# Kernel tuning notes

Measured on AMD Instinct MI355X. Metric: run time of the kernel, lower is better.

The kernel has to match this reference:

```python
import jax, jax.numpy as jnp
import numpy as np

B = 64; WIN_IN = 32; WIN_OUT = 8; NODES = 128; FEAT = 16
HID = 64; LSTM_H = 32; CLASSES = 10
N = B * WIN_IN * NODES      # 262144 total nodes in batched graph
E = 8 * N                   # 2097152 edges (avg degree 8)


def setup_inputs() -> dict:
    key = jax.random.key(0)
    ks = jax.random.split(key, 16)
    p = lambda k, s: (jax.random.normal(k, s, dtype=jnp.float32) * 0.05)
    return {
        "x": jax.random.normal(ks[0], (N, FEAT), dtype=jnp.float32),
        "edge_index": jax.random.randint(ks[1], (2, E), 0, N, dtype=jnp.int32),
        "W1": p(ks[2], (FEAT, HID)),   "b1": p(ks[3], (HID,)),
        "W2": p(ks[4], (HID, FEAT)),   "b2": p(ks[5], (FEAT,)),
        "Wih": p(ks[6], (4 * LSTM_H, NODES * FEAT)),
        "Whh": p(ks[7], (4 * LSTM_H, LSTM_H)),
        "bih": p(ks[8], (4 * LSTM_H,)), "bhh": p(ks[9], (4 * LSTM_H,)),
        "Wfc1": p(ks[10], (16, LSTM_H)), "bfc1": p(ks[11], (16,)),
        "Wfc2": p(ks[12], (CLASSES, 16)), "bfc2": p(ks[13], (CLASSES,)),
    }


def _gcn_conv(x, row, col, W, b):
    # PyG GCNConv: x' = D^-1/2 (A+I) D^-1/2 (x W) + b, deg counted at target (col)
    h = x @ W
    deg = jax.ops.segment_sum(jnp.ones(row.shape[0], jnp.float32), col, num_segments=N) + 1.0
    dinv = jax.lax.rsqrt(deg)
    msg = h[row] * (dinv[row] * dinv[col])[:, None]          # [E, F]
    agg = jax.ops.segment_sum(msg, col, num_segments=N)
    agg = agg + h * (dinv * dinv)[:, None]                   # self-loop term
    return agg + b


def _lstm(seq, Wih, Whh, bih, bhh):
    # seq: [B, T, D] -> outputs [B, T, H]; torch gate order i, f, g, o
    xs = jnp.transpose(seq, (1, 0, 2))
    h0 = jnp.zeros((seq.shape[0], LSTM_H), seq.dtype)
    bias = bih + bhh

    def step(carry, xt):
        h, c = carry
        g = xt @ Wih.T + h @ Whh.T + bias
        i, f, gg, o = jnp.split(g, 4, axis=-1)
        c = jax.nn.sigmoid(f) * c + jax.nn.sigmoid(i) * jnp.tanh(gg)
        h = jax.nn.sigmoid(o) * jnp.tanh(c)
        return (h, c), h

    _, hs = jax.lax.scan(step, (h0, h0), xs)
    return jnp.transpose(hs, (1, 0, 2))


def reference(x, edge_index, W1, b1, W2, b2, Wih, Whh, bih, bhh, Wfc1, bfc1, Wfc2, bfc2):
    row, col = edge_index[0], edge_index[1]
    h = jax.nn.relu(_gcn_conv(x, row, col, W1, b1))
    h = jax.nn.relu(_gcn_conv(h, row, col, W2, b2))
    h = h.reshape(B, WIN_IN, NODES * FEAT)
    h = _lstm(h, Wih, Whh, bih, bhh)
    h = h[:, -WIN_OUT:, :]
    h = jax.nn.relu(h @ Wfc1.T + bfc1)
    h = h @ Wfc2.T + bfc2
    return h.reshape(-1, CLASSES)
```

## Files before the change

### kernel.cpp

```cpp
#include <hip/hip_runtime.h>
#include <hip/hip_fp16.h>

#define NN      262144
#define EDGES   2097152
#define FEATD   16
#define HIDD    64
#define LSTMH   32
#define BATCH   64
#define WIN     32
#define WOUT    8
#define NCLS    10
#define ROWD    2048
#define KCHUNKS 16

#define NB2     512
#define NW      512
#define CAPB    4608
#define NBLK    256
#define CHUNK   (EDGES / NBLK)

__global__ void k_hist(const int* __restrict__ ei, int* __restrict__ hist2d) {
    __shared__ int h[NB2];
    int blk = blockIdx.x, tid = threadIdx.x;
    for (int l = tid; l < NB2; l += 256) h[l] = 0;
    __syncthreads();
    int e0 = blk * CHUNK;
    for (int i = tid; i < CHUNK; i += 256)
        atomicAdd(&h[ei[EDGES + e0 + i] >> 9], 1);
    __syncthreads();
    for (int l = tid; l < NB2; l += 256) hist2d[l * NBLK + blk] = h[l];
}

__global__ void k_scan2(int* __restrict__ hist2d, int* __restrict__ bcnt) {
    __shared__ int s[NBLK];
    int b = blockIdx.x, tid = threadIdx.x;
    int v = hist2d[b * NBLK + tid];
    s[tid] = v;
    __syncthreads();
    for (int off = 1; off < NBLK; off <<= 1) {
        int t = (tid >= off) ? s[tid - off] : 0;
        __syncthreads();
        s[tid] += t;
        __syncthreads();
    }
    hist2d[b * NBLK + tid] = s[tid] - v;
    if (tid == NBLK - 1) bcnt[b] = s[tid];
}

__global__ void k_place(const int* __restrict__ ei, const int* __restrict__ hist2d,
                        int* __restrict__ bdata) {
    __shared__ int curp[NB2];
    int blk = blockIdx.x, tid = threadIdx.x;
    for (int l = tid; l < NB2; l += 256) curp[l] = hist2d[l * NBLK + blk];
    __syncthreads();
    int e0 = blk * CHUNK;
    for (int i = tid; i < CHUNK; i += 256) {
        int r = ei[e0 + i];
        int c = ei[EDGES + e0 + i];
        int b = c >> 9;
        int p = atomicAdd(&curp[b], 1);
        if (p < CAPB) bdata[(size_t)b * CAPB + p] = (r << 9) | (c & 511);
    }
}

__global__ void __launch_bounds__(256)
k_csrsort(const int* __restrict__ bcnt, const int* __restrict__ bdata,
          int* __restrict__ rows, int* __restrict__ off, float* __restrict__ dinv) {
    __shared__ int sidx[CAPB];
    __shared__ int hist[NW], curp[NW];
    int b = blockIdx.x, tid = threadIdx.x;
    int total = bcnt[b]; if (total > CAPB) total = CAPB;
    for (int l = tid; l < NW; l += 256) hist[l] = 0;
    __syncthreads();
    const int* base = bdata + (size_t)b * CAPB;
    for (int i = tid; i < total; i += 256) {
        int w = base[i];
        sidx[i] = w;
        atomicAdd(&hist[w & 511], 1);
    }
    __syncthreads();
    if (tid == 0) {
        int run = 0;
        for (int co = 0; co < NW; co++) { curp[co] = run; run += hist[co]; }
    }
    __syncthreads();
    for (int l = tid; l < NW; l += 256) {
        off[b * NW + l] = curp[l] + hist[l];
        dinv[b * NW + l] = rsqrtf((float)hist[l] + 1.0f);
    }
    __syncthreads();
    for (int i = tid; i < total; i += 256) {
        int w = sidx[i];
        int pos = atomicAdd(&curp[w & 511], 1);
        rows[(size_t)b * CAPB + pos] = w >> 9;
    }
}

__global__ void k_scale(const float* __restrict__ x, const float* __restrict__ dinv,
                        __half2* __restrict__ xsH) {
    int i = blockIdx.x * blockDim.x + threadIdx.x;
    if (i >= NN * 8) return;
    float d = dinv[i >> 3];
    float2 v = ((const float2*)x)[i];
    xsH[i] = __floats2half2_rn(v.x * d, v.y * d);
}

template<int LAYER>
__global__ void __launch_bounds__(256)
k_aggcsr(const int* __restrict__ rows, const int* __restrict__ off,
         const float* __restrict__ dinv, const __half2* __restrict__ srcH,
         const float* __restrict__ b2, __half2* __restrict__ outH) {
    int i = blockIdx.x * blockDim.x + threadIdx.x;
    if (i >= NN * 8) return;
    int n = i >> 3, f2 = i & 7;
    int begin = (n & 511) ? off[n - 1] : 0;
    int end = off[n];
    const size_t base = (size_t)(n >> 9) * CAPB;
    float2 selfv = __half22float2(srcH[(size_t)n * 8 + f2]);
    float ax = selfv.x, ay = selfv.y;
    for (size_t e = base + begin; e < base + end; ++e) {
        int r = rows[e];
        float2 v = __half22float2(srcH[(size_t)r * 8 + f2]);
        ax += v.x; ay += v.y;
    }
    float d = dinv[n];
    ax *= d; ay *= d;
    if (LAYER == 2) {
        ax = fmaxf(ax + b2[f2 * 2 + 0], 0.f);
        ay = fmaxf(ay + b2[f2 * 2 + 1], 0.f);
    }
    outH[i] = __floats2half2_rn(ax, ay);
}

__global__ void k_gcnmlp(const __half2* __restrict__ in1H, __half2* __restrict__ xsH,
                         const float* __restrict__ dinv,
                         const float* __restrict__ W1, const float* __restrict__ b1,
                         const float* __restrict__ W2) {
    __shared__ float sW1[FEATD * HIDD];
    __shared__ float sW2[HIDD * FEATD];
    __shared__ float sb1[HIDD];
    for (int l = threadIdx.x; l < FEATD * HIDD; l += blockDim.x) {
        sW1[l] = W1[l];
        sW2[l] = W2[l];
    }
    if (threadIdx.x < HIDD) sb1[threadIdx.x] = b1[threadIdx.x];
    __syncthreads();
    int n = blockIdx.x * blockDim.x + threadIdx.x;
    if (n >= NN) return;
    union { float4 f4; __half2 h2[4]; } a0, a1;
    a0.f4 = ((const float4*)(in1H + (size_t)n * 8))[0];
    a1.f4 = ((const float4*)(in1H + (size_t)n * 8))[1];
    float in[FEATD];
#pragma unroll
    for (int q = 0; q < 4; q++) {
        float2 v = __half22float2(a0.h2[q]);
        in[q * 2 + 0] = v.x; in[q * 2 + 1] = v.y;
        v = __half22float2(a1.h2[q]);
        in[8 + q * 2 + 0] = v.x; in[8 + q * 2 + 1] = v.y;
    }
    float out[FEATD];
#pragma unroll
    for (int c = 0; c < FEATD; c++) out[c] = 0.f;
#pragma unroll 8
    for (int j = 0; j < HIDD; j++) {
        float h = sb1[j];
#pragma unroll
        for (int f = 0; f < FEATD; f++) h += in[f] * sW1[f * HIDD + j];
        h = fmaxf(h, 0.f);
#pragma unroll
        for (int c = 0; c < FEATD; c++) out[c] += h * sW2[j * FEATD + c];
    }
    float dn = dinv[n];
    union { float4 f4; __half2 h2[4]; } o0, o1;
#pragma unroll
    for (int q = 0; q < 4; q++) {
        o0.h2[q] = __floats2half2_rn(out[q * 2] * dn, out[q * 2 + 1] * dn);
        o1.h2[q] = __floats2half2_rn(out[8 + q * 2] * dn, out[8 + q * 2 + 1] * dn);
    }
    ((float4*)(xsH + (size_t)n * 8))[0] = o0.f4;
    ((float4*)(xsH + (size_t)n * 8))[1] = o1.f4;
}

#define KT 32
#define KSPAN (ROWD / KCHUNKS)
__global__ void __launch_bounds__(256)
k_gemmA(const __half2* __restrict__ h2H, const float* __restrict__ Wih,
        float* __restrict__ gxp) {
    __shared__ float As[16][KT + 2];
    __shared__ float Bs[KT][128 + 4];
    int tid = threadIdx.x;
    int row0 = blockIdx.x * 16;
    int k0 = blockIdx.y * KSPAN;
    int lrow = tid & 15;
    int cb = (tid >> 4) * 8;
    float acc[8];
#pragma unroll
    for (int j = 0; j < 8; j++) acc[j] = 0.f;
    const __half* h2 = (const __half*)h2H;
    for (int kk = 0; kk < KSPAN; kk += KT) {
        if (tid < 64) {
            int rr = tid >> 2, cc = (tid & 3) * 8;
            union { float4 f4; __half2 h2v[4]; } a;
            a.f4 = *(const float4*)(h2 + (size_t)(row0 + rr) * ROWD + k0 + kk + cc);
#pragma unroll
            for (int q = 0; q < 4; q++) {
                float2 v = __half22float2(a.h2v[q]);
                As[rr][cc + q * 2 + 0] = v.x;
                As[rr][cc + q * 2 + 1] = v.y;
            }
        }
#pragma unroll
        for (int w = 0; w < 4; w++) {
            int idx = tid + w * 256;
            int rr = idx >> 3;
            int cc = (idx & 7) * 4;
            float4 v = *(const float4*)&Wih[(size_t)rr * ROWD + k0 + kk + cc];
            Bs[cc + 0][rr] = v.x;
            Bs[cc + 1][rr] = v.y;
            Bs[cc + 2][rr] = v.z;
            Bs[cc + 3][rr] = v.w;
        }
        __syncthreads();
#pragma unroll
        for (int k = 0; k < KT; k++) {
            float a = As[lrow][k];
            float4 b0 = *(const float4*)&Bs[k][cb];
            float4 b1 = *(const float4*)&Bs[k][cb + 4];
            acc[0] += a * b0.x; acc[1] += a * b0.y;
            acc[2] += a * b0.z; acc[3] += a * b0.w;
            acc[4] += a * b1.x; acc[5] += a * b1.y;
            acc[6] += a * b1.z; acc[7] += a * b1.w;
        }
        __syncthreads();
    }
    float* outp = gxp + (size_t)blockIdx.y * (ROWD * 128) + (size_t)(row0 + lrow) * 128 + cb;
    ((float4*)outp)[0] = make_float4(acc[0], acc[1], acc[2], acc[3]);
    ((float4*)outp)[1] = make_float4(acc[4], acc[5], acc[6], acc[7]);
}

__global__ void k_pre(const float* __restrict__ gxp, float* __restrict__ sgx) {
    int i = blockIdx.x * blockDim.x + threadIdx.x;
    if (i >= ROWD * 128) return;
    float s = 0.f;
#pragma unroll
    for (int p = 0; p < KCHUNKS; p++) s += gxp[(size_t)p * ROWD * 128 + i];
    sgx[i] = s;
}

__global__ void k_lstm(const float* __restrict__ sgx, const float* __restrict__ Whh,
                       const float* __restrict__ bih, const float* __restrict__ bhh,
                       float* __restrict__ hseq) {
    __shared__ float sWhhT[LSTMH][4 * LSTMH];
    __shared__ float sgxL[WIN * 4 * LSTMH];
    __shared__ float sh[LSTMH], sc[LSTMH], sg[4 * LSTMH];
    int b = blockIdx.x, j = threadIdx.x;
    for (int l = j; l < 4 * LSTMH * LSTMH; l += 4 * LSTMH) {
        int r = l >> 5, k = l & 31;
        sWhhT[k][r] = Whh[l];
    }
    for (int l = j; l < WIN * 128; l += 128) sgxL[l] = sgx[(size_t)b * WIN * 128 + l];
    float bias = bih[j] + bhh[j];
    if (j < LSTMH) { sh[j] = 0.f; sc[j] = 0.f; }
    __syncthreads();
    for (int t = 0; t < WIN; t++) {
        float g = bias + sgxL[t * 128 + j];
#pragma unroll
        for (int k = 0; k < LSTMH; k++) g += sWhhT[k][j] * sh[k];
        sg[j] = g;
        __syncthreads();
        if (j < LSTMH) {
            float ig = sg[j], fg = sg[32 + j], gg = sg[64 + j], og = sg[96 + j];
            float c = sc[j];
            float si = 1.f / (1.f + __expf(-ig));
            float sf = 1.f / (1.f + __expf(-fg));
            float so = 1.f / (1.f + __expf(-og));
            c = sf * c + si * tanhf(gg);
            float h = so * tanhf(c);
            sc[j] = c; sh[j] = h;
            if (t >= WIN - WOUT)
                hseq[(size_t)(b * WOUT + (t - (WIN - WOUT))) * LSTMH + j] = h;
        }
        __syncthreads();
    }
}

__global__ void k_fc(const float* __restrict__ hseq, const float* __restrict__ Wfc1,
                     const float* __restrict__ bfc1, const float* __restrict__ Wfc2,
                     const float* __restrict__ bfc2, float* __restrict__ out) {
    __shared__ float sW1[16 * 32], sb1[16], sW2[10 * 16], sb2[10];
    int tid = threadIdx.x;
    for (int l = tid; l < 16 * 32; l += blockDim.x) sW1[l] = Wfc1[l];
    if (tid < 16) sb1[tid] = bfc1[tid];
    for (int l = tid; l < 160; l += blockDim.x) sW2[l] = Wfc2[l];
    if (tid < 10) sb2[tid] = bfc2[tid];
    __syncthreads();
    int r = blockIdx.x * blockDim.x + tid;
    if (r >= BATCH * WOUT) return;
    float h[32];
#pragma unroll
    for (int k = 0; k < 32; k++) h[k] = hseq[(size_t)r * 32 + k];
    float hid[16];
#pragma unroll
    for (int j = 0; j < 16; j++) {
        float v = sb1[j];
#pragma unroll
        for (int k = 0; k < 32; k++) v += sW1[j * 32 + k] * h[k];
        hid[j] = fmaxf(v, 0.f);
    }
#pragma unroll
    for (int c = 0; c < NCLS; c++) {
        float v = sb2[c];
#pragma unroll
        for (int j = 0; j < 16; j++) v += sW2[c * 16 + j] * hid[j];
        out[(size_t)r * NCLS + c] = v;
    }
}

extern "C" void kernel_launch(void* const* d_in, const int* in_sizes, int n_in,
                              void* d_out, int out_size, void* d_ws, size_t ws_size,
                              hipStream_t stream) {
    const float* x    = (const float*)d_in[0];
    const int*   ei   = (const int*)d_in[1];
    const float* W1   = (const float*)d_in[2];
    const float* b1   = (const float*)d_in[3];
    const float* W2   = (const float*)d_in[4];
    const float* b2   = (const float*)d_in[5];
    const float* Wih  = (const float*)d_in[6];
    const float* Whh  = (const float*)d_in[7];
    const float* bih  = (const float*)d_in[8];
    const float* bhh  = (const float*)d_in[9];
    const float* Wfc1 = (const float*)d_in[10];
    const float* bfc1 = (const float*)d_in[11];
    const float* Wfc2 = (const float*)d_in[12];
    const float* bfc2 = (const float*)d_in[13];
    float* out = (float*)d_out;

    float*   ws     = (float*)d_ws;
    float*   dinv   = ws;
    int*     hist2d = (int*)(dinv + NN);
    int*     bcnt   = hist2d + NB2 * NBLK;
    int*     off    = bcnt + NB2;
    int*     rows   = off + NN;
    __half2* aggH   = (__half2*)(rows + (size_t)NB2 * CAPB);
    __half2* xsH    = aggH + (size_t)NN * 8;
    int*     bdata  = (int*)(xsH + (size_t)NN * 8);
    float*   gxp    = (float*)(bdata + (size_t)NB2 * CAPB);
    float*   sgx    = gxp + (size_t)KCHUNKS * ROWD * 128;
    float*   hseq   = sgx + ROWD * 128;

    k_hist<<<NBLK, 256, 0, stream>>>(ei, hist2d);
    k_scan2<<<NB2, NBLK, 0, stream>>>(hist2d, bcnt);
    k_place<<<NBLK, 256, 0, stream>>>(ei, hist2d, bdata);
    k_csrsort<<<NB2, 256, 0, stream>>>(bcnt, bdata, rows, off, dinv);
    k_scale<<<NN * 8 / 256, 256, 0, stream>>>(x, dinv, xsH);

    k_aggcsr<1><<<NN * 8 / 256, 256, 0, stream>>>(rows, off, dinv, xsH, b2, aggH);
    k_gcnmlp<<<NN / 256, 256, 0, stream>>>(aggH, xsH, dinv, W1, b1, W2);
    k_aggcsr<2><<<NN * 8 / 256, 256, 0, stream>>>(rows, off, dinv, xsH, b2, aggH);

    dim3 gg(ROWD / 16, KCHUNKS);
    k_gemmA<<<gg, 256, 0, stream>>>(aggH, Wih, gxp);
    k_pre<<<ROWD * 128 / 256, 256, 0, stream>>>(gxp, sgx);
    k_lstm<<<BATCH, 128, 0, stream>>>(sgx, Whh, bih, bhh, hseq);
    k_fc<<<2, 256, 0, stream>>>(hseq, Wfc1, bfc1, Wfc2, bfc2, out);
}
```

Measured before the change: 254.4 us.

## Parallelize CSR sort scan, stage sorted rows in LDS, double GEMM row tile

k_csrsort now runs 512 threads per block. The serial single-thread prefix scan becomes a parallel Hillis-Steele scan, and the scattered global row writes are first placed in shared memory and then written out coalesced. k_gemmA computes 32 rows per block instead of 16, with each thread holding two accumulator sets, so every Wih tile loaded into LDS is reused across twice as many rows and the grid is halved. The cost is more shared memory and registers per block, and lower occupancy and block count for the GEMM.

Result: faster. 235.3 us (-7.5%).

```diff
diff --git a/kernel.cpp b/kernel.cpp
--- a/kernel.cpp
+++ b/kernel.cpp
@@ -63,37 +63,43 @@
     }
 }
 
-__global__ void __launch_bounds__(256)
+__global__ void __launch_bounds__(512)
 k_csrsort(const int* __restrict__ bcnt, const int* __restrict__ bdata,
-          int* __restrict__ rows, int* __restrict__ off, float* __restrict__ dinv) {
+          int* __restrict__ rows, int* __restrict__ offp, float* __restrict__ dinv) {
     __shared__ int sidx[CAPB];
-    __shared__ int hist[NW], curp[NW];
+    __shared__ int sorted[CAPB];
+    __shared__ int hist[NW], curp[NW], ssc[NW];
     int b = blockIdx.x, tid = threadIdx.x;
     int total = bcnt[b]; if (total > CAPB) total = CAPB;
-    for (int l = tid; l < NW; l += 256) hist[l] = 0;
+    hist[tid] = 0;
     __syncthreads();
     const int* base = bdata + (size_t)b * CAPB;
-    for (int i = tid; i < total; i += 256) {
+    for (int i = tid; i < total; i += 512) {
         int w = base[i];
         sidx[i] = w;
         atomicAdd(&hist[w & 511], 1);
     }
     __syncthreads();
-    if (tid == 0) {
-        int run = 0;
-        for (int co = 0; co < NW; co++) { curp[co] = run; run += hist[co]; }
-    }
-    __syncthreads();
-    for (int l = tid; l < NW; l += 256) {
-        off[b * NW + l] = curp[l] + hist[l];
-        dinv[b * NW + l] = rsqrtf((float)hist[l] + 1.0f);
-    }
-    __syncthreads();
-    for (int i = tid; i < total; i += 256) {
+    int v = hist[tid];
+    ssc[tid] = v;
+    __syncthreads();
+    for (int st = 1; st < NW; st <<= 1) {
+        int t = (tid >= st) ? ssc[tid - st] : 0;
+        __syncthreads();
+        ssc[tid] += t;
+        __syncthreads();
+    }
+    curp[tid] = ssc[tid] - v;
+    offp[b * NW + tid] = ssc[tid];
+    dinv[b * NW + tid] = rsqrtf((float)v + 1.0f);
+    __syncthreads();
+    for (int i = tid; i < total; i += 512) {
         int w = sidx[i];
         int pos = atomicAdd(&curp[w & 511], 1);
-        rows[(size_t)b * CAPB + pos] = w >> 9;
-    }
+        sorted[pos] = w >> 9;
+    }
+    __syncthreads();
+    for (int i = tid; i < total; i += 512) rows[(size_t)b * CAPB + i] = sorted[i];
 }
 
 __global__ void k_scale(const float* __restrict__ x, const float* __restrict__ dinv,
@@ -186,19 +192,19 @@
 __global__ void __launch_bounds__(256)
 k_gemmA(const __half2* __restrict__ h2H, const float* __restrict__ Wih,
         float* __restrict__ gxp) {
-    __shared__ float As[16][KT + 2];
+    __shared__ float As[32][KT + 2];
     __shared__ float Bs[KT][128 + 4];
     int tid = threadIdx.x;
-    int row0 = blockIdx.x * 16;
+    int row0 = blockIdx.x * 32;
     int k0 = blockIdx.y * KSPAN;
-    int lrow = tid & 15;
+    int r0 = tid & 15, r1 = r0 + 16;
     int cb = (tid >> 4) * 8;
-    float acc[8];
-#pragma unroll
-    for (int j = 0; j < 8; j++) acc[j] = 0.f;
+    float acc0[8], acc1[8];
+#pragma unroll
+    for (int j = 0; j < 8; j++) { acc0[j] = 0.f; acc1[j] = 0.f; }
     const __half* h2 = (const __half*)h2H;
     for (int kk = 0; kk < KSPAN; kk += KT) {
-        if (tid < 64) {
+        if (tid < 128) {
             int rr = tid >> 2, cc = (tid & 3) * 8;
             union { float4 f4; __half2 h2v[4]; } a;
             a.f4 = *(const float4*)(h2 + (size_t)(row0 + rr) * ROWD + k0 + kk + cc);
@@ -223,19 +229,27 @@
         __syncthreads();
 #pragma unroll
         for (int k = 0; k < KT; k++) {
-            float a = As[lrow][k];
+            float a0 = As[r0][k];
+            float a1 = As[r1][k];
             float4 b0 = *(const float4*)&Bs[k][cb];
             float4 b1 = *(const float4*)&Bs[k][cb + 4];
-            acc[0] += a * b0.x; acc[1] += a * b0.y;
-            acc[2] += a * b0.z; acc[3] += a * b0.w;
-            acc[4] += a * b1.x; acc[5] += a * b1.y;
-            acc[6] += a * b1.z; acc[7] += a * b1.w;
+            acc0[0] += a0 * b0.x; acc0[1] += a0 * b0.y;
+            acc0[2] += a0 * b0.z; acc0[3] += a0 * b0.w;
+            acc0[4] += a0 * b1.x; acc0[5] += a0 * b1.y;
+            acc0[6] += a0 * b1.z; acc0[7] += a0 * b1.w;
+            acc1[0] += a1 * b0.x; acc1[1] += a1 * b0.y;
+            acc1[2] += a1 * b0.z; acc1[3] += a1 * b0.w;
+            acc1[4] += a1 * b1.x; acc1[5] += a1 * b1.y;
+            acc1[6] += a1 * b1.z; acc1[7] += a1 * b1.w;
         }
         __syncthreads();
     }
-    float* outp = gxp + (size_t)blockIdx.y * (ROWD * 128) + (size_t)(row0 + lrow) * 128 + cb;
-    ((float4*)outp)[0] = make_float4(acc[0], acc[1], acc[2], acc[3]);
-    ((float4*)outp)[1] = make_float4(acc[4], acc[5], acc[6], acc[7]);
+    float* o0 = gxp + (size_t)blockIdx.y * (ROWD * 128) + (size_t)(row0 + r0) * 128 + cb;
+    float* o1 = gxp + (size_t)blockIdx.y * (ROWD * 128) + (size_t)(row0 + r1) * 128 + cb;
+    ((float4*)o0)[0] = make_float4(acc0[0], acc0[1], acc0[2], acc0[3]);
+    ((float4*)o0)[1] = make_float4(acc0[4], acc0[5], acc0[6], acc0[7]);
+    ((float4*)o1)[0] = make_float4(acc1[0], acc1[1], acc1[2], acc1[3]);
+    ((float4*)o1)[1] = make_float4(acc1[4], acc1[5], acc1[6], acc1[7]);
 }
 
 __global__ void k_pre(const float* __restrict__ gxp, float* __restrict__ sgx) {
@@ -351,14 +365,14 @@
     k_hist<<<NBLK, 256, 0, stream>>>(ei, hist2d);
     k_scan2<<<NB2, NBLK, 0, stream>>>(hist2d, bcnt);
     k_place<<<NBLK, 256, 0, stream>>>(ei, hist2d, bdata);
-    k_csrsort<<<NB2, 256, 0, stream>>>(bcnt, bdata, rows, off, dinv);
+    k_csrsort<<<NB2, 512, 0, stream>>>(bcnt, bdata, rows, off, dinv);
     k_scale<<<NN * 8 / 256, 256, 0, stream>>>(x, dinv, xsH);
 
     k_aggcsr<1><<<NN * 8 / 256, 256, 0, stream>>>(rows, off, dinv, xsH, b2, aggH);
     k_gcnmlp<<<NN / 256, 256, 0, stream>>>(aggH, xsH, dinv, W1, b1, W2);
     k_aggcsr<2><<<NN * 8 / 256, 256, 0, stream>>>(rows, off, dinv, xsH, b2, aggH);
 
-    dim3 gg(ROWD / 16, KCHUNKS);
+    dim3 gg(ROWD / 32, KCHUNKS);
     k_gemmA<<<gg, 256, 0, stream>>>(aggH, Wih, gxp);
     k_pre<<<ROWD * 128 / 256, 256, 0, stream>>>(gxp, sgx);
     k_lstm<<<BATCH, 128, 0, stream>>>(sgx, Whh, bih, bhh, hseq);
```
